# Kernel tuning notes

Hardware: AMD Instinct MI355X
Metric: run time of the kernel (lower is better)

Reference implementation:

```python
import jax, jax.numpy as jnp
import numpy as np

DIMS = [2048, 2048, 2048, 2048, 1000]
BATCH = 1024
N_RELAX = 25
RELAX_LR = 0.3
N_LAYERS = len(DIMS) - 1  # 4 weight matrices, states indexed 0..4


def setup_inputs() -> dict:
    key = jax.random.key(0)
    ks = jax.random.split(key, N_LAYERS + 1)
    inp = {"x": jax.random.normal(ks[0], (BATCH, DIMS[0]), jnp.float32)}
    for i in range(N_LAYERS):
        scale = np.float32(np.sqrt(2.0 / DIMS[i]))
        inp[f"W{i}"] = jax.random.normal(ks[i + 1], (DIMS[i], DIMS[i + 1]), jnp.float32) * scale
    # biases[0] is never used in forward; biases[1..4] init to zeros as in torch code
    for l in range(1, N_LAYERS + 1):
        inp[f"b{l}"] = jnp.zeros((DIMS[l],), jnp.float32)
    return inp


def _rho(t):
    return jnp.clip(t, 0.0, 1.0)


def _relax(x, Ws, bs):
    # bs[l-1] corresponds to original biases[l] (state l's bias), l = 1..N_LAYERS
    # feedforward initialization pass
    states = [x]
    h = x
    for l in range(N_LAYERS):
        h = _rho(h @ Ws[l] + bs[l])
        states.append(h)

    # Gauss-Seidel sweep: states[l-1] already updated this iteration when l uses it
    def sweep(carry, _):
        full = [x] + list(carry)
        for l in range(1, N_LAYERS + 1):
            ds = -full[l] + bs[l - 1] + _rho(full[l - 1]) @ Ws[l - 1]
            if l < N_LAYERS:
                ds = ds + _rho(full[l + 1]) @ Ws[l].T
            full[l] = _rho(full[l] + RELAX_LR * ds)
        return tuple(full[1:]), None

    carry, _ = jax.lax.scan(sweep, tuple(states[1:]), None, length=N_RELAX)
    return carry


def reference(x, W0, W1, W2, W3, b1, b2, b3, b4):
    Ws = [W0, W1, W2, W3]
    bs = [b1, b2, b3, b4]
    states = _relax(x, Ws, bs)
    return states[-1]  # [BATCH, DIMS[-1]]
```

## Files before the change

### kernel.cpp

```cpp
#include <hip/hip_runtime.h>
#include <hip/hip_bf16.h>

typedef _Float16 fp16_t;
typedef _Float16 v8h __attribute__((ext_vector_type(8)));
typedef float    v4f __attribute__((ext_vector_type(4)));

#define RELAX_LR 0.3f

__device__ __forceinline__ void async_cp16(const void* g, void* l) {
    __builtin_amdgcn_global_load_lds(
        (const __attribute__((address_space(1))) void*)g,
        (__attribute__((address_space(3))) void*)l, 16, 0, 0);
}

__global__ __launch_bounds__(256, 2) void gemm_splitk_kernel(
    const fp16_t* __restrict__ A1, const fp16_t* __restrict__ B1t, int K1, int CK1, int nz1,
    const fp16_t* __restrict__ A2, const fp16_t* __restrict__ B2t, int K2s, int CK2,
    fp16_t* __restrict__ part, int Ntot)
{
    __shared__ __align__(16) fp16_t As[2][2][128][32];
    __shared__ __align__(16) fp16_t Bs[2][2][128][32];

    const int tid  = threadIdx.x;
    const int lane = tid & 63;
    const int w    = tid >> 6;
    const int wm   = w >> 1;
    const int wn   = w & 1;
    const int quad = lane >> 4;
    const int lrow = lane & 15;

    const int blk  = blockIdx.x;
    const int low3 = blk & 7;
    const int g    = blk >> 3;
    const int bm   = g & 7;
    const int c    = (g >> 3) * 8 + low3;
    int bn, z;
    if (Ntot == 2048) { bn = c >> 2; z = c & 3; }
    else              { bn = c >> 3; z = c & 7; }

    const fp16_t *A, *Bt; int stride, koff, CK;
    if (z < nz1) { A = A1; Bt = B1t; stride = K1;  CK = CK1; koff = z * CK1; }
    else         { A = A2; Bt = B2t; stride = K2s; CK = CK2; koff = (z - nz1) * CK2; }

    const int sr = lane >> 2;
    const int sc = (lane & 3) * 8;
    const fp16_t* ag = A  + (size_t)(bm * 128 + 32 * w + sr) * stride + koff + sc;
    const fp16_t* bg = Bt + (size_t)(bn * 128 + 32 * w + sr) * stride + koff + sc;
    const size_t st16 = (size_t)16 * stride;

    v4f acc[4][4] = {};
    const int iters = CK >> 6;

    auto stage = [&](int buf, int kb) {
        const fp16_t* a0 = ag + kb;
        const fp16_t* b0 = bg + kb;
        async_cp16(a0,             &As[buf][0][32 * w     ][0]);
        async_cp16(a0 + st16,      &As[buf][0][32 * w + 16][0]);
        async_cp16(a0 + 32,        &As[buf][1][32 * w     ][0]);
        async_cp16(a0 + 32 + st16, &As[buf][1][32 * w + 16][0]);
        async_cp16(b0,             &Bs[buf][0][32 * w     ][0]);
        async_cp16(b0 + st16,      &Bs[buf][0][32 * w + 16][0]);
        async_cp16(b0 + 32,        &Bs[buf][1][32 * w     ][0]);
        async_cp16(b0 + 32 + st16, &Bs[buf][1][32 * w + 16][0]);
    };

    stage(0, 0);

    for (int it = 0; it < iters; ++it) {
        __syncthreads();
        if (it + 1 < iters) stage((it + 1) & 1, (it + 1) * 64);
        const int cur = it & 1;
        #pragma unroll
        for (int h = 0; h < 2; ++h) {
            v8h af[4], bv[4];
            #pragma unroll
            for (int fm = 0; fm < 4; ++fm)
                af[fm] = *(const v8h*)&As[cur][h][wm * 64 + fm * 16 + lrow][quad * 8];
            #pragma unroll
            for (int fn = 0; fn < 4; ++fn)
                bv[fn] = *(const v8h*)&Bs[cur][h][wn * 64 + fn * 16 + lrow][quad * 8];
            #pragma unroll
            for (int fm = 0; fm < 4; ++fm)
                #pragma unroll
                for (int fn = 0; fn < 4; ++fn)
                    acc[fm][fn] = __builtin_amdgcn_mfma_f32_16x16x32_f16(
                        af[fm], bv[fn], acc[fm][fn], 0, 0, 0);
        }
    }

    fp16_t* po = part + (size_t)z * 1024 * Ntot;
    const int rowbase = bm * 128 + wm * 64 + quad * 4;
    const int colbase = bn * 128 + wn * 64;
    #pragma unroll
    for (int fn = 0; fn < 4; ++fn) {
        const int col = colbase + fn * 16 + lrow;
        #pragma unroll
        for (int fm = 0; fm < 4; ++fm) {
            const int row = rowbase + fm * 16;
            #pragma unroll
            for (int r = 0; r < 4; ++r)
                po[(size_t)(row + r) * Ntot + col] = (fp16_t)acc[fm][fn][r];
        }
    }
}

__global__ __launch_bounds__(256) void reduce_update_kernel(
    const fp16_t* __restrict__ part, int nz,
    const float* __restrict__ bias, const float* __restrict__ extra,
    const fp16_t* s_old, fp16_t* outb,
    int Ntot, int do_update, int total8, float* __restrict__ finout)
{
    const int i = blockIdx.x * 256 + threadIdx.x;
    if (i >= total8) return;
    const size_t e = (size_t)i * 8;

    float v[8];
    {
        const v8h p0 = *(const v8h*)(part + e);
        #pragma unroll
        for (int j = 0; j < 8; ++j) v[j] = (float)p0[j];
    }
    for (int z = 1; z < nz; ++z) {
        const v8h p = *(const v8h*)(part + (size_t)z * 1024 * Ntot + e);
        #pragma unroll
        for (int j = 0; j < 8; ++j) v[j] += (float)p[j];
    }
    const int col = (int)e & (Ntot - 1);
    if (extra) {
        const float4 e0 = *(const float4*)(extra + e);
        const float4 e1 = *(const float4*)(extra + e + 4);
        v[0] += e0.x; v[1] += e0.y; v[2] += e0.z; v[3] += e0.w;
        v[4] += e1.x; v[5] += e1.y; v[6] += e1.z; v[7] += e1.w;
    } else {
        const float4 b0 = *(const float4*)(bias + col);
        const float4 b1 = *(const float4*)(bias + col + 4);
        v[0] += b0.x; v[1] += b0.y; v[2] += b0.z; v[3] += b0.w;
        v[4] += b1.x; v[5] += b1.y; v[6] += b1.z; v[7] += b1.w;
    }
    if (do_update) {
        const v8h so = *(const v8h*)(s_old + e);
        #pragma unroll
        for (int j = 0; j < 8; ++j) {
            const float s = (float)so[j];
            v[j] = s + RELAX_LR * (v[j] - s);
        }
    }
    #pragma unroll
    for (int j = 0; j < 8; ++j) v[j] = fminf(fmaxf(v[j], 0.f), 1.f);
    v8h h;
    #pragma unroll
    for (int j = 0; j < 8; ++j) h[j] = (fp16_t)v[j];
    *(v8h*)(outb + e) = h;

    if (finout && col < 1000) {
        const int row = (int)(e >> 10);
        float* o = finout + (size_t)row * 1000 + col;
        float4 o0 = {v[0], v[1], v[2], v[3]};
        float4 o1 = {v[4], v[5], v[6], v[7]};
        *(float4*)o       = o0;
        *(float4*)(o + 4) = o1;
    }
}

__global__ __launch_bounds__(256) void makec1_kernel(
    const fp16_t* __restrict__ part, const float* __restrict__ bias,
    float* __restrict__ c1f, int total8)
{
    const int i = blockIdx.x * 256 + threadIdx.x;
    if (i >= total8) return;
    const size_t e = (size_t)i * 8;
    float v[8];
    {
        const v8h p0 = *(const v8h*)(part + e);
        #pragma unroll
        for (int j = 0; j < 8; ++j) v[j] = (float)p0[j];
    }
    #pragma unroll
    for (int z = 1; z < 4; ++z) {
        const v8h p = *(const v8h*)(part + (size_t)z * 1024 * 2048 + e);
        #pragma unroll
        for (int j = 0; j < 8; ++j) v[j] += (float)p[j];
    }
    const int col = (int)e & 2047;
    const float4 b0 = *(const float4*)(bias + col);
    const float4 b1 = *(const float4*)(bias + col + 4);
    v[0] += b0.x; v[1] += b0.y; v[2] += b0.z; v[3] += b0.w;
    v[4] += b1.x; v[5] += b1.y; v[6] += b1.z; v[7] += b1.w;
    float4 o0 = {v[0], v[1], v[2], v[3]};
    float4 o1 = {v[4], v[5], v[6], v[7]};
    *(float4*)(c1f + e)     = o0;
    *(float4*)(c1f + e + 4) = o1;
}

__global__ void conv_w_kernel(const float* __restrict__ W, int R, int C,
                              fp16_t* Wb, fp16_t* __restrict__ WbT,
                              int Rp, int Cp)
{
    __shared__ float t[32][33];
    const int tx = threadIdx.x & 31;
    const int ty = threadIdx.x >> 5;
    const int r0 = blockIdx.y * 32;
    const int c0 = blockIdx.x * 32;
    #pragma unroll
    for (int i = 0; i < 4; ++i) {
        const int r = r0 + ty + i * 8;
        const int c = c0 + tx;
        float v = 0.f;
        if (r < R && c < C) v = W[(size_t)r * C + c];
        t[ty + i * 8][tx] = v;
    }
    __syncthreads();
    if (Wb) {
        #pragma unroll
        for (int i = 0; i < 4; ++i) {
            const int r = r0 + ty + i * 8;
            const int c = c0 + tx;
            if (r < Rp && c < Cp) Wb[(size_t)r * Cp + c] = (fp16_t)t[ty + i * 8][tx];
        }
    }
    #pragma unroll
    for (int i = 0; i < 4; ++i) {
        const int cc = c0 + ty + i * 8;
        const int rr = r0 + tx;
        if (cc < Cp && rr < Rp) WbT[(size_t)cc * Rp + rr] = (fp16_t)t[tx][ty + i * 8];
    }
}

__global__ void conv_x_kernel(const float* __restrict__ x,
                              fp16_t* __restrict__ xb, fp16_t* __restrict__ rxb, int n)
{
    const int i = blockIdx.x * blockDim.x + threadIdx.x;
    if (i < n) {
        const float v = x[i];
        xb[i]  = (fp16_t)v;
        rxb[i] = (fp16_t)fminf(fmaxf(v, 0.f), 1.f);
    }
}

__global__ void pad_b4_kernel(const float* __restrict__ b4, float* __restrict__ b4p)
{
    const int i = blockIdx.x * blockDim.x + threadIdx.x;
    if (i < 1024) b4p[i] = (i < 1000) ? b4[i] : 0.f;
}

extern "C" void kernel_launch(void* const* d_in, const int* in_sizes, int n_in,
                              void* d_out, int out_size, void* d_ws, size_t ws_size,
                              hipStream_t stream)
{
    const float* x  = (const float*)d_in[0];
    const float* W0 = (const float*)d_in[1];
    const float* W1 = (const float*)d_in[2];
    const float* W2 = (const float*)d_in[3];
    const float* W3 = (const float*)d_in[4];
    const float* b1 = (const float*)d_in[5];
    const float* b2 = (const float*)d_in[6];
    const float* b3 = (const float*)d_in[7];
    const float* b4 = (const float*)d_in[8];
    float* out = (float*)d_out;

    char* p = (char*)d_ws;
    auto alloc = [&](size_t bytes) {
        char* q = p;
        p += (bytes + 255) & ~(size_t)255;
        return q;
    };

    fp16_t* xb   = (fp16_t*)alloc((size_t)1024 * 2048 * 2);
    fp16_t* rxb  = (fp16_t*)alloc((size_t)1024 * 2048 * 2);
    fp16_t* Wb1  = (fp16_t*)alloc((size_t)2048 * 2048 * 2);
    fp16_t* Wb2  = (fp16_t*)alloc((size_t)2048 * 2048 * 2);
    fp16_t* Wb3  = (fp16_t*)alloc((size_t)2048 * 1024 * 2);
    fp16_t* WbT0 = (fp16_t*)alloc((size_t)2048 * 2048 * 2);
    fp16_t* WbT1 = (fp16_t*)alloc((size_t)2048 * 2048 * 2);
    fp16_t* WbT2 = (fp16_t*)alloc((size_t)2048 * 2048 * 2);
    fp16_t* WbT3 = (fp16_t*)alloc((size_t)1024 * 2048 * 2);
    fp16_t* s1b  = (fp16_t*)alloc((size_t)1024 * 2048 * 2);
    fp16_t* s2b  = (fp16_t*)alloc((size_t)1024 * 2048 * 2);
    fp16_t* s3b  = (fp16_t*)alloc((size_t)1024 * 2048 * 2);
    fp16_t* s4b  = (fp16_t*)alloc((size_t)1024 * 1024 * 2);
    float*  b4p  = (float*)alloc(1024 * 4);
    float*  c1f  = (float*)alloc((size_t)1024 * 2048 * 4);
    fp16_t* part = (fp16_t*)alloc((size_t)4 * 1024 * 2048 * 2);
    (void)ws_size; (void)in_sizes; (void)n_in; (void)out_size;

    conv_x_kernel<<<(1024 * 2048 + 255) / 256, 256, 0, stream>>>(x, xb, rxb, 1024 * 2048);
    pad_b4_kernel<<<4, 256, 0, stream>>>(b4, b4p);
    conv_w_kernel<<<dim3(64, 64), 256, 0, stream>>>(W0, 2048, 2048, nullptr, WbT0, 2048, 2048);
    conv_w_kernel<<<dim3(64, 64), 256, 0, stream>>>(W1, 2048, 2048, Wb1, WbT1, 2048, 2048);
    conv_w_kernel<<<dim3(64, 64), 256, 0, stream>>>(W2, 2048, 2048, Wb2, WbT2, 2048, 2048);
    conv_w_kernel<<<dim3(32, 64), 256, 0, stream>>>(W3, 2048, 1000, Wb3, WbT3, 2048, 1024);

    const dim3 blk(256);
    const dim3 g512(512);
    const int t8_2048 = 1024 * 2048 / 8;
    const int t8_1024 = 1024 * 1024 / 8;
    const int rg2048 = t8_2048 / 256;
    const int rg1024 = t8_1024 / 256;

    gemm_splitk_kernel<<<g512, blk, 0, stream>>>(rxb, WbT0, 2048, 512, 4, nullptr, nullptr, 0, 0, part, 2048);
    makec1_kernel<<<rg2048, blk, 0, stream>>>(part, b1, c1f, t8_2048);

    gemm_splitk_kernel<<<g512, blk, 0, stream>>>(xb,  WbT0, 2048, 512, 4, nullptr, nullptr, 0, 0, part, 2048);
    reduce_update_kernel<<<rg2048, blk, 0, stream>>>(part, 4, b1, nullptr, nullptr, s1b, 2048, 0, t8_2048, nullptr);
    gemm_splitk_kernel<<<g512, blk, 0, stream>>>(s1b, WbT1, 2048, 512, 4, nullptr, nullptr, 0, 0, part, 2048);
    reduce_update_kernel<<<rg2048, blk, 0, stream>>>(part, 4, b2, nullptr, nullptr, s2b, 2048, 0, t8_2048, nullptr);
    gemm_splitk_kernel<<<g512, blk, 0, stream>>>(s2b, WbT2, 2048, 512, 4, nullptr, nullptr, 0, 0, part, 2048);
    reduce_update_kernel<<<rg2048, blk, 0, stream>>>(part, 4, b3, nullptr, nullptr, s3b, 2048, 0, t8_2048, nullptr);
    gemm_splitk_kernel<<<g512, blk, 0, stream>>>(s3b, WbT3, 2048, 256, 8, nullptr, nullptr, 0, 0, part, 1024);
    reduce_update_kernel<<<rg1024, blk, 0, stream>>>(part, 8, b4p, nullptr, nullptr, s4b, 1024, 0, t8_1024, nullptr);

    for (int it = 0; it < 25; ++it) {
        gemm_splitk_kernel<<<g512, blk, 0, stream>>>(s2b, Wb1, 2048, 512, 4, nullptr, nullptr, 0, 0, part, 2048);
        reduce_update_kernel<<<rg2048, blk, 0, stream>>>(part, 4, nullptr, c1f, s1b, s1b, 2048, 1, t8_2048, nullptr);
        gemm_splitk_kernel<<<g512, blk, 0, stream>>>(s1b, WbT1, 2048, 1024, 2, s3b, Wb2, 2048, 1024, part, 2048);
        reduce_update_kernel<<<rg2048, blk, 0, stream>>>(part, 4, b2, nullptr, s2b, s2b, 2048, 1, t8_2048, nullptr);
        gemm_splitk_kernel<<<g512, blk, 0, stream>>>(s2b, WbT2, 2048, 1024, 2, s4b, Wb3, 1024, 512, part, 2048);
        reduce_update_kernel<<<rg2048, blk, 0, stream>>>(part, 4, b3, nullptr, s3b, s3b, 2048, 1, t8_2048, nullptr);
        gemm_splitk_kernel<<<g512, blk, 0, stream>>>(s3b, WbT3, 2048, 256, 8, nullptr, nullptr, 0, 0, part, 1024);
        reduce_update_kernel<<<rg1024, blk, 0, stream>>>(part, 8, b4p, nullptr, s4b, s4b, 1024, 1, t8_1024,
                                                         (it == 24) ? out : nullptr);
    }
}
```

Baseline: 2.757 ms.

## Co-launch layer-4 and next-iteration layer-1 GEMMs and balance split-K chunks

The GEMM and reduce kernels now take two job descriptors and a block split point, so one launch can serve two independent jobs. The layer-4 update of one sweep and the layer-1 update of the next sweep depend on different states, so they are merged into a single GEMM launch and a single reduce launch. This cuts launches per sweep from eight to six and fills the GPU with more concurrent work. The layer-3 job now treats its two products as one concatenated K range split into equal chunks, rather than unequal halves, to balance work across blocks. Separate partial-sum buffers are added so the merged jobs do not overwrite each other, at the cost of extra memory and some per-block job selection logic.

```diff
diff --git a/kernel.cpp b/kernel.cpp
--- a/kernel.cpp
+++ b/kernel.cpp
@@ -13,10 +13,13 @@
         (__attribute__((address_space(3))) void*)l, 16, 0, 0);
 }
 
-__global__ __launch_bounds__(256, 2) void gemm_splitk_kernel(
-    const fp16_t* __restrict__ A1, const fp16_t* __restrict__ B1t, int K1, int CK1, int nz1,
-    const fp16_t* __restrict__ A2, const fp16_t* __restrict__ B2t, int K2s, int CK2,
-    fp16_t* __restrict__ part, int Ntot)
+struct GJob {
+    const fp16_t *A1, *B1t, *A2, *B2t;
+    fp16_t* part;
+    int K1, K2s, CK, Ntot;
+};
+
+__global__ __launch_bounds__(256, 2) void gemm_splitk_kernel(GJob j0, GJob j1, int nb0)
 {
     __shared__ __align__(16) fp16_t As[2][2][128][32];
     __shared__ __align__(16) fp16_t Bs[2][2][128][32];
@@ -29,46 +32,52 @@
     const int quad = lane >> 4;
     const int lrow = lane & 15;
 
-    const int blk  = blockIdx.x;
-    const int low3 = blk & 7;
-    const int g    = blk >> 3;
+    int bblk = blockIdx.x;
+    const GJob j = (bblk < nb0) ? j0 : j1;
+    if (bblk >= nb0) bblk -= nb0;
+
+    const int low3 = bblk & 7;
+    const int g    = bblk >> 3;
     const int bm   = g & 7;
     const int c    = (g >> 3) * 8 + low3;
     int bn, z;
-    if (Ntot == 2048) { bn = c >> 2; z = c & 3; }
-    else              { bn = c >> 3; z = c & 7; }
-
-    const fp16_t *A, *Bt; int stride, koff, CK;
-    if (z < nz1) { A = A1; Bt = B1t; stride = K1;  CK = CK1; koff = z * CK1; }
-    else         { A = A2; Bt = B2t; stride = K2s; CK = CK2; koff = (z - nz1) * CK2; }
+    if (j.Ntot == 2048) { bn = c >> 2; z = c & 3; }
+    else                { bn = c >> 3; z = c & 7; }
+    const int k0 = z * j.CK;
 
     const int sr = lane >> 2;
     const int sc = (lane & 3) * 8;
-    const fp16_t* ag = A  + (size_t)(bm * 128 + 32 * w + sr) * stride + koff + sc;
-    const fp16_t* bg = Bt + (size_t)(bn * 128 + 32 * w + sr) * stride + koff + sc;
-    const size_t st16 = (size_t)16 * stride;
+    const size_t rowA = (size_t)(bm * 128 + 32 * w + sr);
+    const size_t rowB = (size_t)(bn * 128 + 32 * w + sr);
+    const fp16_t* a1 = j.A1  + rowA * j.K1 + sc;
+    const fp16_t* b1 = j.B1t + rowB * j.K1 + sc;
+    const fp16_t* a2 = j.A2  ? j.A2  + rowA * j.K2s + sc : nullptr;
+    const fp16_t* b2 = j.B2t ? j.B2t + rowB * j.K2s + sc : nullptr;
+    const size_t s16a = (size_t)16 * j.K1;
+    const size_t s16b = (size_t)16 * j.K2s;
+
+    auto stage = [&](int buf, int kc) {
+        const fp16_t *a0, *b0; size_t st;
+        if (kc < j.K1) { a0 = a1 + kc;          b0 = b1 + kc;          st = s16a; }
+        else           { a0 = a2 + (kc - j.K1); b0 = b2 + (kc - j.K1); st = s16b; }
+        async_cp16(a0,           &As[buf][0][32 * w     ][0]);
+        async_cp16(a0 + st,      &As[buf][0][32 * w + 16][0]);
+        async_cp16(a0 + 32,      &As[buf][1][32 * w     ][0]);
+        async_cp16(a0 + 32 + st, &As[buf][1][32 * w + 16][0]);
+        async_cp16(b0,           &Bs[buf][0][32 * w     ][0]);
+        async_cp16(b0 + st,      &Bs[buf][0][32 * w + 16][0]);
+        async_cp16(b0 + 32,      &Bs[buf][1][32 * w     ][0]);
+        async_cp16(b0 + 32 + st, &Bs[buf][1][32 * w + 16][0]);
+    };
 
     v4f acc[4][4] = {};
-    const int iters = CK >> 6;
-
-    auto stage = [&](int buf, int kb) {
-        const fp16_t* a0 = ag + kb;
-        const fp16_t* b0 = bg + kb;
-        async_cp16(a0,             &As[buf][0][32 * w     ][0]);
-        async_cp16(a0 + st16,      &As[buf][0][32 * w + 16][0]);
-        async_cp16(a0 + 32,        &As[buf][1][32 * w     ][0]);
-        async_cp16(a0 + 32 + st16, &As[buf][1][32 * w + 16][0]);
-        async_cp16(b0,             &Bs[buf][0][32 * w     ][0]);
-        async_cp16(b0 + st16,      &Bs[buf][0][32 * w + 16][0]);
-        async_cp16(b0 + 32,        &Bs[buf][1][32 * w     ][0]);
-        async_cp16(b0 + 32 + st16, &Bs[buf][1][32 * w + 16][0]);
-    };
-
-    stage(0, 0);
+    const int iters = j.CK >> 6;
+
+    stage(0, k0);
 
     for (int it = 0; it < iters; ++it) {
         __syncthreads();
-        if (it + 1 < iters) stage((it + 1) & 1, (it + 1) * 64);
+        if (it + 1 < iters) stage((it + 1) & 1, k0 + (it + 1) * 64);
         const int cur = it & 1;
         #pragma unroll
         for (int h = 0; h < 2; ++h) {
@@ -88,7 +97,7 @@
         }
     }
 
-    fp16_t* po = part + (size_t)z * 1024 * Ntot;
+    fp16_t* po = j.part + (size_t)z * 1024 * j.Ntot;
     const int rowbase = bm * 128 + wm * 64 + quad * 4;
     const int colbase = bn * 128 + wn * 64;
     #pragma unroll
@@ -99,62 +108,69 @@
             const int row = rowbase + fm * 16;
             #pragma unroll
             for (int r = 0; r < 4; ++r)
-                po[(size_t)(row + r) * Ntot + col] = (fp16_t)acc[fm][fn][r];
-        }
-    }
-}
-
-__global__ __launch_bounds__(256) void reduce_update_kernel(
-    const fp16_t* __restrict__ part, int nz,
-    const float* __restrict__ bias, const float* __restrict__ extra,
-    const fp16_t* s_old, fp16_t* outb,
-    int Ntot, int do_update, int total8, float* __restrict__ finout)
-{
-    const int i = blockIdx.x * 256 + threadIdx.x;
-    if (i >= total8) return;
-    const size_t e = (size_t)i * 8;
+                po[(size_t)(row + r) * j.Ntot + col] = (fp16_t)acc[fm][fn][r];
+        }
+    }
+}
+
+struct RJob {
+    const fp16_t* part;
+    const float* bias;
+    const float* extra;
+    const fp16_t* s_old;
+    fp16_t* outb;
+    float* finout;
+    int nz, Ntot, do_update;
+};
+
+__global__ __launch_bounds__(256) void reduce_update_kernel(RJob j0, RJob j1, int nb0)
+{
+    int b = blockIdx.x;
+    const RJob j = (b < nb0) ? j0 : j1;
+    if (b >= nb0) b -= nb0;
+    const size_t e = ((size_t)b * 256 + threadIdx.x) * 8;
 
     float v[8];
     {
-        const v8h p0 = *(const v8h*)(part + e);
-        #pragma unroll
-        for (int j = 0; j < 8; ++j) v[j] = (float)p0[j];
-    }
-    for (int z = 1; z < nz; ++z) {
-        const v8h p = *(const v8h*)(part + (size_t)z * 1024 * Ntot + e);
-        #pragma unroll
-        for (int j = 0; j < 8; ++j) v[j] += (float)p[j];
-    }
-    const int col = (int)e & (Ntot - 1);
-    if (extra) {
-        const float4 e0 = *(const float4*)(extra + e);
-        const float4 e1 = *(const float4*)(extra + e + 4);
+        const v8h p0 = *(const v8h*)(j.part + e);
+        #pragma unroll
+        for (int k = 0; k < 8; ++k) v[k] = (float)p0[k];
+    }
+    for (int z = 1; z < j.nz; ++z) {
+        const v8h p = *(const v8h*)(j.part + (size_t)z * 1024 * j.Ntot + e);
+        #pragma unroll
+        for (int k = 0; k < 8; ++k) v[k] += (float)p[k];
+    }
+    const int col = (int)e & (j.Ntot - 1);
+    if (j.extra) {
+        const float4 e0 = *(const float4*)(j.extra + e);
+        const float4 e1 = *(const float4*)(j.extra + e + 4);
         v[0] += e0.x; v[1] += e0.y; v[2] += e0.z; v[3] += e0.w;
         v[4] += e1.x; v[5] += e1.y; v[6] += e1.z; v[7] += e1.w;
     } else {
-        const float4 b0 = *(const float4*)(bias + col);
-        const float4 b1 = *(const float4*)(bias + col + 4);
+        const float4 b0 = *(const float4*)(j.bias + col);
+        const float4 b1 = *(const float4*)(j.bias + col + 4);
         v[0] += b0.x; v[1] += b0.y; v[2] += b0.z; v[3] += b0.w;
         v[4] += b1.x; v[5] += b1.y; v[6] += b1.z; v[7] += b1.w;
     }
-    if (do_update) {
-        const v8h so = *(const v8h*)(s_old + e);
-        #pragma unroll
-        for (int j = 0; j < 8; ++j) {
-            const float s = (float)so[j];
-            v[j] = s + RELAX_LR * (v[j] - s);
-        }
-    }
-    #pragma unroll
-    for (int j = 0; j < 8; ++j) v[j] = fminf(fmaxf(v[j], 0.f), 1.f);
+    if (j.do_update) {
+        const v8h so = *(const v8h*)(j.s_old + e);
+        #pragma unroll
+        for (int k = 0; k < 8; ++k) {
+            const float s = (float)so[k];
+            v[k] = s + RELAX_LR * (v[k] - s);
+        }
+    }
+    #pragma unroll
+    for (int k = 0; k < 8; ++k) v[k] = fminf(fmaxf(v[k], 0.f), 1.f);
     v8h h;
     #pragma unroll
-    for (int j = 0; j < 8; ++j) h[j] = (fp16_t)v[j];
-    *(v8h*)(outb + e) = h;
-
-    if (finout && col < 1000) {
+    for (int k = 0; k < 8; ++k) h[k] = (fp16_t)v[k];
+    *(v8h*)(j.outb + e) = h;
+
+    if (j.finout && col < 1000) {
         const int row = (int)(e >> 10);
-        float* o = finout + (size_t)row * 1000 + col;
+        float* o = j.finout + (size_t)row * 1000 + col;
         float4 o0 = {v[0], v[1], v[2], v[3]};
         float4 o1 = {v[4], v[5], v[6], v[7]};
         *(float4*)o       = o0;
@@ -173,13 +189,13 @@
     {
         const v8h p0 = *(const v8h*)(part + e);
         #pragma unroll
-        for (int j = 0; j < 8; ++j) v[j] = (float)p0[j];
+        for (int k = 0; k < 8; ++k) v[k] = (float)p0[k];
     }
     #pragma unroll
     for (int z = 1; z < 4; ++z) {
         const v8h p = *(const v8h*)(part + (size_t)z * 1024 * 2048 + e);
         #pragma unroll
-        for (int j = 0; j < 8; ++j) v[j] += (float)p[j];
+        for (int k = 0; k < 8; ++k) v[k] += (float)p[k];
     }
     const int col = (int)e & 2047;
     const float4 b0 = *(const float4*)(bias + col);
@@ -265,22 +281,23 @@
         return q;
     };
 
-    fp16_t* xb   = (fp16_t*)alloc((size_t)1024 * 2048 * 2);
-    fp16_t* rxb  = (fp16_t*)alloc((size_t)1024 * 2048 * 2);
-    fp16_t* Wb1  = (fp16_t*)alloc((size_t)2048 * 2048 * 2);
-    fp16_t* Wb2  = (fp16_t*)alloc((size_t)2048 * 2048 * 2);
-    fp16_t* Wb3  = (fp16_t*)alloc((size_t)2048 * 1024 * 2);
-    fp16_t* WbT0 = (fp16_t*)alloc((size_t)2048 * 2048 * 2);
-    fp16_t* WbT1 = (fp16_t*)alloc((size_t)2048 * 2048 * 2);
-    fp16_t* WbT2 = (fp16_t*)alloc((size_t)2048 * 2048 * 2);
-    fp16_t* WbT3 = (fp16_t*)alloc((size_t)1024 * 2048 * 2);
-    fp16_t* s1b  = (fp16_t*)alloc((size_t)1024 * 2048 * 2);
-    fp16_t* s2b  = (fp16_t*)alloc((size_t)1024 * 2048 * 2);
-    fp16_t* s3b  = (fp16_t*)alloc((size_t)1024 * 2048 * 2);
-    fp16_t* s4b  = (fp16_t*)alloc((size_t)1024 * 1024 * 2);
-    float*  b4p  = (float*)alloc(1024 * 4);
-    float*  c1f  = (float*)alloc((size_t)1024 * 2048 * 4);
-    fp16_t* part = (fp16_t*)alloc((size_t)4 * 1024 * 2048 * 2);
+    fp16_t* xb    = (fp16_t*)alloc((size_t)1024 * 2048 * 2);
+    fp16_t* rxb   = (fp16_t*)alloc((size_t)1024 * 2048 * 2);
+    fp16_t* Wb1   = (fp16_t*)alloc((size_t)2048 * 2048 * 2);
+    fp16_t* Wb2   = (fp16_t*)alloc((size_t)2048 * 2048 * 2);
+    fp16_t* Wb3   = (fp16_t*)alloc((size_t)2048 * 1024 * 2);
+    fp16_t* WbT0  = (fp16_t*)alloc((size_t)2048 * 2048 * 2);
+    fp16_t* WbT1  = (fp16_t*)alloc((size_t)2048 * 2048 * 2);
+    fp16_t* WbT2  = (fp16_t*)alloc((size_t)2048 * 2048 * 2);
+    fp16_t* WbT3  = (fp16_t*)alloc((size_t)1024 * 2048 * 2);
+    fp16_t* s1b   = (fp16_t*)alloc((size_t)1024 * 2048 * 2);
+    fp16_t* s2b   = (fp16_t*)alloc((size_t)1024 * 2048 * 2);
+    fp16_t* s3b   = (fp16_t*)alloc((size_t)1024 * 2048 * 2);
+    fp16_t* s4b   = (fp16_t*)alloc((size_t)1024 * 1024 * 2);
+    float*  b4p   = (float*)alloc(1024 * 4);
+    float*  c1f   = (float*)alloc((size_t)1024 * 2048 * 4);
+    fp16_t* partA = (fp16_t*)alloc((size_t)8 * 1024 * 1024 * 2);
+    fp16_t* partB = (fp16_t*)alloc((size_t)4 * 1024 * 2048 * 2);
     (void)ws_size; (void)in_sizes; (void)n_in; (void)out_size;
 
     conv_x_kernel<<<(1024 * 2048 + 255) / 256, 256, 0, stream>>>(x, xb, rxb, 1024 * 2048);
@@ -291,33 +308,54 @@
     conv_w_kernel<<<dim3(32, 64), 256, 0, stream>>>(W3, 2048, 1000, Wb3, WbT3, 2048, 1024);
 
     const dim3 blk(256);
-    const dim3 g512(512);
-    const int t8_2048 = 1024 * 2048 / 8;
-    const int t8_1024 = 1024 * 1024 / 8;
-    const int rg2048 = t8_2048 / 256;
-    const int rg1024 = t8_1024 / 256;
-
-    gemm_splitk_kernel<<<g512, blk, 0, stream>>>(rxb, WbT0, 2048, 512, 4, nullptr, nullptr, 0, 0, part, 2048);
-    makec1_kernel<<<rg2048, blk, 0, stream>>>(part, b1, c1f, t8_2048);
-
-    gemm_splitk_kernel<<<g512, blk, 0, stream>>>(xb,  WbT0, 2048, 512, 4, nullptr, nullptr, 0, 0, part, 2048);
-    reduce_update_kernel<<<rg2048, blk, 0, stream>>>(part, 4, b1, nullptr, nullptr, s1b, 2048, 0, t8_2048, nullptr);
-    gemm_splitk_kernel<<<g512, blk, 0, stream>>>(s1b, WbT1, 2048, 512, 4, nullptr, nullptr, 0, 0, part, 2048);
-    reduce_update_kernel<<<rg2048, blk, 0, stream>>>(part, 4, b2, nullptr, nullptr, s2b, 2048, 0, t8_2048, nullptr);
-    gemm_splitk_kernel<<<g512, blk, 0, stream>>>(s2b, WbT2, 2048, 512, 4, nullptr, nullptr, 0, 0, part, 2048);
-    reduce_update_kernel<<<rg2048, blk, 0, stream>>>(part, 4, b3, nullptr, nullptr, s3b, 2048, 0, t8_2048, nullptr);
-    gemm_splitk_kernel<<<g512, blk, 0, stream>>>(s3b, WbT3, 2048, 256, 8, nullptr, nullptr, 0, 0, part, 1024);
-    reduce_update_kernel<<<rg1024, blk, 0, stream>>>(part, 8, b4p, nullptr, nullptr, s4b, 1024, 0, t8_1024, nullptr);
-
+    const int rg2048 = 1024 * 2048 / 8 / 256;
+    const int rg1024 = 1024 * 1024 / 8 / 256;
+
+    const GJob jC1 = { rxb, WbT0, nullptr, nullptr, partA, 2048, 0,    512,  2048 };
+    const GJob jI1 = { xb,  WbT0, nullptr, nullptr, partB, 2048, 0,    512,  2048 };
+    const GJob jI2 = { s1b, WbT1, nullptr, nullptr, partB, 2048, 0,    512,  2048 };
+    const GJob jI3 = { s2b, WbT2, nullptr, nullptr, partB, 2048, 0,    512,  2048 };
+    const GJob jI4 = { s3b, WbT3, nullptr, nullptr, partA, 2048, 0,    256,  1024 };
+    const GJob jL1 = { s2b, Wb1,  nullptr, nullptr, partB, 2048, 0,    512,  2048 };
+    const GJob jL2 = { s1b, WbT1, s3b, Wb2,         partB, 2048, 2048, 1024, 2048 };
+    const GJob jL3 = { s2b, WbT2, s4b, Wb3,         partB, 2048, 1024, 768,  2048 };
+    const GJob jL4 = { s3b, WbT3, nullptr, nullptr, partA, 2048, 0,    256,  1024 };
+
+    const RJob rI1 = { partB, b1,  nullptr, nullptr, s1b, nullptr, 4, 2048, 0 };
+    const RJob rI2 = { partB, b2,  nullptr, nullptr, s2b, nullptr, 4, 2048, 0 };
+    const RJob rI3 = { partB, b3,  nullptr, nullptr, s3b, nullptr, 4, 2048, 0 };
+    const RJob rI4 = { partA, b4p, nullptr, nullptr, s4b, nullptr, 8, 1024, 0 };
+    const RJob rL1 = { partB, nullptr, c1f, s1b, s1b, nullptr, 4, 2048, 1 };
+    const RJob rL2 = { partB, b2,  nullptr, s2b, s2b, nullptr, 4, 2048, 1 };
+    const RJob rL3 = { partB, b3,  nullptr, s3b, s3b, nullptr, 4, 2048, 1 };
+    const RJob rL4 = { partA, b4p, nullptr, s4b, s4b, nullptr, 8, 1024, 1 };
+    RJob rL4f = rL4; rL4f.finout = out;
+
+    gemm_splitk_kernel<<<512, blk, 0, stream>>>(jC1, jC1, 512);
+    makec1_kernel<<<rg2048, blk, 0, stream>>>(partA, b1, c1f, 1024 * 2048 / 8);
+
+    gemm_splitk_kernel<<<512, blk, 0, stream>>>(jI1, jI1, 512);
+    reduce_update_kernel<<<rg2048, blk, 0, stream>>>(rI1, rI1, rg2048);
+    gemm_splitk_kernel<<<512, blk, 0, stream>>>(jI2, jI2, 512);
+    reduce_update_kernel<<<rg2048, blk, 0, stream>>>(rI2, rI2, rg2048);
+    gemm_splitk_kernel<<<512, blk, 0, stream>>>(jI3, jI3, 512);
+    reduce_update_kernel<<<rg2048, blk, 0, stream>>>(rI3, rI3, rg2048);
+    gemm_splitk_kernel<<<512, blk, 0, stream>>>(jI4, jI4, 512);
+    reduce_update_kernel<<<rg1024, blk, 0, stream>>>(rI4, rI4, rg1024);
+
+    gemm_splitk_kernel<<<512, blk, 0, stream>>>(jL1, jL1, 512);
+    reduce_update_kernel<<<rg2048, blk, 0, stream>>>(rL1, rL1, rg2048);
     for (int it = 0; it < 25; ++it) {
-        gemm_splitk_kernel<<<g512, blk, 0, stream>>>(s2b, Wb1, 2048, 512, 4, nullptr, nullptr, 0, 0, part, 2048);
-        reduce_update_kernel<<<rg2048, blk, 0, stream>>>(part, 4, nullptr, c1f, s1b, s1b, 2048, 1, t8_2048, nullptr);
-        gemm_splitk_kernel<<<g512, blk, 0, stream>>>(s1b, WbT1, 2048, 1024, 2, s3b, Wb2, 2048, 1024, part, 2048);
-        reduce_update_kernel<<<rg2048, blk, 0, stream>>>(part, 4, b2, nullptr, s2b, s2b, 2048, 1, t8_2048, nullptr);
-        gemm_splitk_kernel<<<g512, blk, 0, stream>>>(s2b, WbT2, 2048, 1024, 2, s4b, Wb3, 1024, 512, part, 2048);
-        reduce_update_kernel<<<rg2048, blk, 0, stream>>>(part, 4, b3, nullptr, s3b, s3b, 2048, 1, t8_2048, nullptr);
-        gemm_splitk_kernel<<<g512, blk, 0, stream>>>(s3b, WbT3, 2048, 256, 8, nullptr, nullptr, 0, 0, part, 1024);
-        reduce_update_kernel<<<rg1024, blk, 0, stream>>>(part, 8, b4p, nullptr, s4b, s4b, 1024, 1, t8_1024,
-                                                         (it == 24) ? out : nullptr);
-    }
-}
+        gemm_splitk_kernel<<<512, blk, 0, stream>>>(jL2, jL2, 512);
+        reduce_update_kernel<<<rg2048, blk, 0, stream>>>(rL2, rL2, rg2048);
+        gemm_splitk_kernel<<<512, blk, 0, stream>>>(jL3, jL3, 512);
+        reduce_update_kernel<<<rg2048, blk, 0, stream>>>(rL3, rL3, rg2048);
+        if (it < 24) {
+            gemm_splitk_kernel<<<1024, blk, 0, stream>>>(jL4, jL1, 512);
+            reduce_update_kernel<<<rg1024 + rg2048, blk, 0, stream>>>(rL4, rL1, rg1024);
+        } else {
+            gemm_splitk_kernel<<<512, blk, 0, stream>>>(jL4, jL4, 512);
+            reduce_update_kernel<<<rg1024, blk, 0, stream>>>(rL4f, rL4f, rg1024);
+        }
+    }
+}
```

New measurement: 2.412 ms. 12.5% less time.
